# Kernel optimization log

Hardware: AMD Instinct MI355X
Metric: run time of the kernel (lower is better)

## Reference

```python
import jax, jax.numpy as jnp
import numpy as np

B, H, G, N, D, S, K = 1, 32, 128, 64, 128, 256, 8
BIT_PACK = 8


def setup_inputs() -> dict:
    key = jax.random.key(0)
    ks = jax.random.split(key, 6)
    data = jax.random.normal(ks[0], (B, H, G, N, D), dtype=jnp.float32)
    query = jax.random.normal(ks[1], (B, H, 1, D), dtype=jnp.float32)
    outlier_indices = jax.random.randint(ks[2], (B, H, G, K), 0, D, dtype=jnp.int32)
    norm_data = jax.random.uniform(ks[3], (B, H, G, N), dtype=jnp.float32)
    norm_outlier = jax.random.uniform(ks[4], (B, H, G, N), dtype=jnp.float32)
    # _init_proj_dir + _init_rot_dir (rot=True): per-chunk QR, scaled by sqrt(D)
    proj = np.asarray(jax.random.normal(ks[5], (D, S), dtype=jnp.float32), dtype=np.float64)
    num_chunks = (S + D - 1) // D
    qs = []
    for i in range(num_chunks):
        q, _ = np.linalg.qr(proj[:, i * D:(i + 1) * D])
        qs.append(q)
    proj_dir_score = jnp.asarray(np.concatenate(qs, axis=-1) * np.sqrt(D), dtype=jnp.float32)  # [D, S]
    proj_dir_quant = proj_dir_score.T  # [S, D]
    return {"data": data, "query": query, "outlier_indices": outlier_indices,
            "norm_data": norm_data, "norm_outlier": norm_outlier,
            "proj_dir_quant": proj_dir_quant, "proj_dir_score": proj_dir_score}


def _pack_bits(sketched):
    # sketched: [..., S] -> uint8 packed [..., S//8] ; bit = (sketched > 0)
    x = (sketched > 0).astype(jnp.int32).reshape(*sketched.shape[:-1], -1, BIT_PACK)
    enc = (2 ** jnp.arange(BIT_PACK, dtype=jnp.int32))
    return (x * enc).sum(axis=-1).astype(jnp.uint8)


def reference(data, query, outlier_indices, norm_data, norm_outlier, proj_dir_quant, proj_dir_score):
    s = proj_dir_quant.shape[0]
    d = data.shape[-1]
    # scatter outlier indices into a {0,1} mask over head_dim, per (B,H,G)
    mask = (jax.nn.one_hot(outlier_indices, d, dtype=jnp.float32).sum(axis=-2) > 0).astype(data.dtype)  # [B,H,G,D]
    key_outlier = data * mask[..., None, :]
    key_inlier = data * (1.0 - mask)[..., None, :]
    # JL random projection: [B,H,G,N,D] x [S,D] -> [B,H,G,N,S]
    sk_outlier = jnp.einsum('bhgnd,sd->bhgns', key_outlier, proj_dir_quant)
    sk_inlier = jnp.einsum('bhgnd,sd->bhgns', key_inlier, proj_dir_quant)
    # 1-bit sign quantization + byte packing
    hash_inlier = _pack_bits(sk_inlier)                  # [B,H,G,N,S//8]
    hash_outlier = _pack_bits(sk_outlier)[..., : s // 16]  # truncated outlier sketch
    # score path (PyTorch fallback math): inlier hamming-style inner product
    sketched_q = jnp.einsum('bhqd,ds->bhqs', query, proj_dir_score)[:, :, 0, :]  # [B,H,S]
    bits = jnp.where(sk_inlier > 0, 1.0, -1.0).astype(jnp.float32)  # == unpacked hash_inlier bits *2-1
    ip = jnp.einsum('bhs,bhgns->bhgn', sketched_q, bits)
    scl = jnp.sqrt(jnp.asarray(np.pi / 2, dtype=jnp.float32)) / s
    scores = (scl * norm_data * ip).reshape(data.shape[0], data.shape[1], -1, 1)  # [B,H,G*N,1]
    return hash_inlier, hash_outlier, scores
```

## Files before the change

### kernel.cpp

```cpp
#include <hip/hip_runtime.h>
#include <hip/hip_bf16.h>


typedef __attribute__((ext_vector_type(8))) short short8;
typedef __attribute__((ext_vector_type(4))) float f32x4;

constexpr int cH = 32, cG = 128, cN = 64, cD = 128, cS = 256, cK = 8;
constexpr int HASH_OUT_BASE = cH * cG * cN * (cS / 8);
constexpr int SCORE_BASE    = HASH_OUT_BASE + cH * cG * cN * (cS / 16);
constexpr float EPS_IN  = 1e-3f;
constexpr float EPS_OUT = 1e-3f;
constexpr size_t WS_BHI = 32768, WS_BLO = 98304, WS_NEED = 163840;

#define MFMA(a, b, c) __builtin_amdgcn_mfma_f32_16x16x32_bf16(a, b, c, 0, 0, 0)

__device__ inline short f2bf(float x) {
    unsigned u = __builtin_bit_cast(unsigned, x);
    u += 0x7FFFu + ((u >> 16) & 1u);
    return (short)(u >> 16);
}
__device__ inline float bf2f(short s) {
    return __builtin_bit_cast(float, (unsigned)((unsigned short)s) << 16);
}
__device__ inline unsigned long long sel4(unsigned long long a0, unsigned long long a1,
                                          unsigned long long a2, unsigned long long a3, int r) {
    unsigned long long x = a0;
    x = (r == 1) ? a1 : x; x = (r == 2) ? a2 : x; x = (r == 3) ? a3 : x;
    return x;
}
__device__ inline int sel8(const int* u, int k) {
    int x = u[0];
    x = (k == 1) ? u[1] : x; x = (k == 2) ? u[2] : x; x = (k == 3) ? u[3] : x;
    x = (k == 4) ? u[4] : x; x = (k == 5) ? u[5] : x; x = (k == 6) ? u[6] : x;
    x = (k == 7) ? u[7] : x;
    return x;
}
#define CE(i, j) { int a = u[i], b = u[j]; u[i] = min(a, b); u[j] = max(a, b); }

__device__ __attribute__((noinline)) float exact_inlier(
    const float* __restrict__ dr, const float* __restrict__ pr,
    unsigned long long m0, unsigned long long m1)
{
    float ex = 0.0f;
    #pragma unroll 1
    for (int dc = 0; dc < 4; ++dc) {
        float4 da[8], pa[8];
        #pragma unroll
        for (int j = 0; j < 8; ++j) {
            da[j] = reinterpret_cast<const float4*>(dr)[dc * 8 + j];
            pa[j] = reinterpret_cast<const float4*>(pr)[dc * 8 + j];
        }
        #pragma unroll
        for (int j = 0; j < 8; ++j) {
            float dv[4] = { da[j].x, da[j].y, da[j].z, da[j].w };
            float pv[4] = { pa[j].x, pa[j].y, pa[j].z, pa[j].w };
            #pragma unroll
            for (int e = 0; e < 4; ++e) {
                const int d = dc * 32 + j * 4 + e;
                const bool msk = ((((d < 64) ? (m0 >> d) : (m1 >> (d - 64))) & 1ull) != 0);
                ex = fmaf(dv[e], msk ? 0.0f : pv[e], ex);
            }
        }
    }
    return ex;
}

__global__ __launch_bounds__(256) void qjl_qv(
    const float* __restrict__ query, const float* __restrict__ projs,
    float* __restrict__ qv_out)
{
    const int h = blockIdx.x, s = threadIdx.x;
    float qa = 0.0f;
    for (int d = 0; d < cD; ++d)
        qa = fmaf(query[h * cD + d], projs[d * cS + s], qa);
    qv_out[h * cS + s] = qa;
}

__global__ __launch_bounds__(256) void qjl_bfrag(
    const float* __restrict__ projq, short* __restrict__ bhi, short* __restrict__ blo)
{
    const int idx = blockIdx.x * 256 + threadIdx.x;
    const int l = idx & 63, nt = (idx >> 6) & 15, ksub = idx >> 10;
    const int s = nt * 16 + (l & 15);
    const int k0 = ksub * 32 + (l >> 4) * 8;
    #pragma unroll
    for (int j = 0; j < 8; ++j) {
        float x = projq[s * cD + k0 + j];
        short h = f2bf(x);
        bhi[idx * 8 + j] = h;
        blo[idx * 8 + j] = f2bf(x - bf2f(h));
    }
}

__global__ __launch_bounds__(256, 3) void qjl_mfma(
    const float* __restrict__ data, const int* __restrict__ oidx,
    const float* __restrict__ norm_data, const float* __restrict__ projq,
    const float* __restrict__ qv_ws, const short* __restrict__ bhi_ws,
    const short* __restrict__ blo_ws, float* __restrict__ out)
{
    const int b    = blockIdx.x;
    const int t    = threadIdx.x;
    const int lane = t & 63;
    const int w    = t >> 6;
    const int c0   = lane & 15;
    const int g16  = lane >> 4;
    const int h    = b >> 7;

    __shared__ short A_hi[16 * 64 * 8];
    __shared__ short A_lo[16 * 64 * 8];
    __shared__ float dO[cK * cN];
    __shared__ float pO[cK * cS];
    __shared__ float ipPart[cN * 4];

    const f32x4 zero4 = { 0.f, 0.f, 0.f, 0.f };

    int u[cK];
    #pragma unroll
    for (int k = 0; k < cK; ++k) u[k] = oidx[b * cK + k];
    unsigned long long m0 = 0, m1 = 0;
    #pragma unroll
    for (int k = 0; k < cK; ++k) {
        int v = u[k];
        if (v < 64) m0 |= 1ull << v; else m1 |= 1ull << (v - 64);
    }
    CE(0,1) CE(2,3) CE(4,5) CE(6,7)
    CE(0,2) CE(1,3) CE(4,6) CE(5,7)
    CE(1,2) CE(5,6)
    CE(0,4) CE(1,5) CE(2,6) CE(3,7)
    CE(2,4) CE(3,5)
    CE(1,2) CE(3,4) CE(5,6)

    const float* __restrict__ chunk = data + (size_t)b * (cN * cD);

    #pragma unroll
    for (int i = 0; i < 4; ++i) {
        const int slot = i * 256 + t;
        const int l = slot & 63, frag = slot >> 6;
        const int mt = frag & 3, ksub = frag >> 2;
        const int row = mt * 16 + (l & 15);
        const int k0 = ksub * 32 + (l >> 4) * 8;
        const float4* p = reinterpret_cast<const float4*>(chunk + row * cD + k0);
        float4 v0 = p[0], v1 = p[1];
        float xs[8] = { v0.x, v0.y, v0.z, v0.w, v1.x, v1.y, v1.z, v1.w };
        const unsigned bits = (unsigned)(((k0 < 64) ? (m0 >> k0) : (m1 >> (k0 - 64))) & 0xFFull);
        short hs[8], ls[8];
        #pragma unroll
        for (int e = 0; e < 8; ++e) {
            float x = ((bits >> e) & 1u) ? 0.0f : xs[e];
            hs[e] = f2bf(x);
            ls[e] = f2bf(x - bf2f(hs[e]));
        }
        *reinterpret_cast<short8*>(&A_hi[slot * 8]) =
            short8{ hs[0], hs[1], hs[2], hs[3], hs[4], hs[5], hs[6], hs[7] };
        *reinterpret_cast<short8*>(&A_lo[slot * 8]) =
            short8{ ls[0], ls[1], ls[2], ls[3], ls[4], ls[5], ls[6], ls[7] };
    }
    #pragma unroll
    for (int i = 0; i < 2; ++i) {
        const int idx = i * 256 + t;
        const int k = idx >> 6, row = idx & 63;
        dO[idx] = chunk[row * cD + sel8(u, k)];
    }
    #pragma unroll
    for (int i = 0; i < 8; ++i) {
        const int idx = i * 256 + t;
        const int k = idx >> 8, s = idx & 255;
        const int uk = sel8(u, k);
        const bool dup = (k > 0) && (uk == sel8(u, k - 1));
        float x = projq[s * cD + uk];
        pO[idx] = dup ? 0.0f : x;
    }
    __syncthreads();

    if (w < 2) {
        short8 aO[4];
        #pragma unroll
        for (int mt = 0; mt < 4; ++mt) {
            short v8[8];
            #pragma unroll
            for (int k = 0; k < cK; ++k) {
                float x = dO[k * cN + mt * 16 + c0];
                short hi = f2bf(x), lo = f2bf(x - bf2f(hi));
                v8[k] = (g16 == 2) ? lo : ((g16 == 3) ? (short)0 : hi);
            }
            aO[mt] = short8{ v8[0], v8[1], v8[2], v8[3], v8[4], v8[5], v8[6], v8[7] };
        }
        short8 bO[4];
        #pragma unroll
        for (int q = 0; q < 4; ++q) {
            const int s = (w * 4 + q) * 16 + c0;
            short v8[8];
            #pragma unroll
            for (int k = 0; k < cK; ++k) {
                float x = pO[k * cS + s];
                short hi = f2bf(x), lo = f2bf(x - bf2f(hi));
                v8[k] = (g16 == 1) ? lo : ((g16 == 3) ? (short)0 : hi);
            }
            bO[q] = short8{ v8[0], v8[1], v8[2], v8[3], v8[4], v8[5], v8[6], v8[7] };
        }
        #pragma unroll
        for (int mt = 0; mt < 4; ++mt) {
            #pragma unroll
            for (int q = 0; q < 4; ++q) {
                f32x4 accO = MFMA(aO[mt], bO[q], zero4);
                unsigned long long b0, b1, b2, b3;
                #pragma unroll
                for (int r = 0; r < 4; ++r) {
                    float v = accO[r];
                    if (fabsf(v) < EPS_OUT) {
                        int row = mt * 16 + 4 * g16 + r;
                        int s = (w * 4 + q) * 16 + c0;
                        float o = 0.0f;
                        #pragma unroll
                        for (int k = 0; k < cK; ++k)
                            o = fmaf(dO[k * cN + row], pO[k * cS + s], o);
                        v = o;
                    }
                    unsigned long long bal = __ballot(v > 0.0f);
                    if (r == 0) b0 = bal; else if (r == 1) b1 = bal;
                    else if (r == 2) b2 = bal; else b3 = bal;
                }
                if (lane < 32) {
                    int r = lane & 3, g = (lane >> 2) & 3, hb = lane >> 4;
                    unsigned long long bb = sel4(b0, b1, b2, b3, r);
                    int row = mt * 16 + 4 * g + r;
                    out[HASH_OUT_BASE + (size_t)b * (cN * 16) + row * 16 + (w * 4 + q) * 2 + hb] =
                        (float)((bb >> (16 * g + 8 * hb)) & 0xFFull);
                }
            }
        }
    }

    f32x4 acc[16];
    #pragma unroll
    for (int i = 0; i < 16; ++i)
        acc[i] = zero4;

    #pragma unroll
    for (int ksub = 0; ksub < 4; ++ksub) {
        short8 ah[4], al[4];
        #pragma unroll
        for (int mt = 0; mt < 4; ++mt) {
            ah[mt] = *reinterpret_cast<const short8*>(&A_hi[((ksub * 4 + mt) * 64 + lane) * 8]);
            al[mt] = *reinterpret_cast<const short8*>(&A_lo[((ksub * 4 + mt) * 64 + lane) * 8]);
        }
        #pragma unroll
        for (int q = 0; q < 4; ++q) {
            short8 bh = *reinterpret_cast<const short8*>(
                &bhi_ws[((ksub * 16 + w * 4 + q) * 64 + lane) * 8]);
            #pragma unroll
            for (int mt = 0; mt < 4; ++mt)
                acc[mt * 4 + q] = MFMA(ah[mt], bh, acc[mt * 4 + q]);
            short8 bl = *reinterpret_cast<const short8*>(
                &blo_ws[((ksub * 16 + w * 4 + q) * 64 + lane) * 8]);
            #pragma unroll
            for (int mt = 0; mt < 4; ++mt)
                acc[mt * 4 + q] = MFMA(ah[mt], bl, acc[mt * 4 + q]);
            #pragma unroll
            for (int mt = 0; mt < 4; ++mt)
                acc[mt * 4 + q] = MFMA(al[mt], bh, acc[mt * 4 + q]);
        }
    }

    float qvv[4];
    #pragma unroll
    for (int q = 0; q < 4; ++q)
        qvv[q] = qv_ws[h * cS + (w * 4 + q) * 16 + c0];

    #pragma unroll
    for (int mt = 0; mt < 4; ++mt) {
        float part[4] = { 0.f, 0.f, 0.f, 0.f };
        #pragma unroll
        for (int q = 0; q < 4; ++q) {
            unsigned long long b0, b1, b2, b3;
            #pragma unroll
            for (int r = 0; r < 4; ++r) {
                float v = acc[mt * 4 + q][r];
                if (fabsf(v) < EPS_IN) {
                    int row = mt * 16 + 4 * g16 + r;
                    int s = (w * 4 + q) * 16 + c0;
                    v = exact_inlier(chunk + row * cD, projq + s * cD, m0, m1);
                }
                bool bit = v > 0.0f;
                unsigned long long bal = __ballot(bit);
                part[r] += bit ? qvv[q] : -qvv[q];
                if (r == 0) b0 = bal; else if (r == 1) b1 = bal;
                else if (r == 2) b2 = bal; else b3 = bal;
            }
            if (lane < 32) {
                int r = lane & 3, g = (lane >> 2) & 3, hb = lane >> 4;
                unsigned long long bb = sel4(b0, b1, b2, b3, r);
                int row = mt * 16 + 4 * g + r;
                out[(size_t)b * (cN * 32) + row * 32 + (w * 4 + q) * 2 + hb] =
                    (float)((bb >> (16 * g + 8 * hb)) & 0xFFull);
            }
        }
        #pragma unroll
        for (int r = 0; r < 4; ++r) {
            float x = part[r];
            x += __shfl_xor(x, 1); x += __shfl_xor(x, 2);
            x += __shfl_xor(x, 4); x += __shfl_xor(x, 8);
            if (c0 == 0) ipPart[(mt * 16 + 4 * g16 + r) * 4 + w] = x;
        }
    }
    __syncthreads();
    if (t < cN) {
        float ip = ipPart[t * 4 + 0] + ipPart[t * 4 + 1]
                 + ipPart[t * 4 + 2] + ipPart[t * 4 + 3];
        const float scl = 0.0048957583f;
        out[SCORE_BASE + (size_t)b * cN + t] = scl * norm_data[b * cN + t] * ip;
    }
}

__global__ __launch_bounds__(256) void qjl_valu(
    const float* __restrict__ data, const float* __restrict__ query,
    const int* __restrict__ oidx, const float* __restrict__ norm_data,
    const float* __restrict__ projq, const float* __restrict__ projs,
    float* __restrict__ out)
{
    const int b2 = blockIdx.x, b = b2 >> 1, half = b2 & 1;
    const int t = threadIdx.x, lane = t & 63, w = t >> 6, h = b >> 7;
    __shared__ float ipPart[32 * 4];
    int u[cK]; int U = 0;
    for (int k = 0; k < cK; ++k) {
        int v = oidx[b * cK + k];
        bool dup = false;
        for (int j = 0; j < U; ++j) dup = dup || (u[j] == v);
        if (!dup) u[U++] = v;
    }
    for (int i = 1; i < U; ++i) {
        int key = u[i], j = i - 1;
        while (j >= 0 && u[j] > key) { u[j + 1] = u[j]; --j; }
        u[j + 1] = key;
    }
    unsigned long long m0 = 0, m1 = 0;
    for (int k = 0; k < U; ++k) {
        int v = u[k];
        if (v < 64) m0 |= 1ull << v; else m1 |= 1ull << (v - 64);
    }
    int ui[cK]; float prO[cK];
    #pragma unroll
    for (int k = 0; k < cK; ++k) ui[k] = (k < U) ? u[k] : 0;
    #pragma unroll
    for (int k = 0; k < cK; ++k) prO[k] = (k < U) ? projq[t * cD + ui[k]] : 0.0f;
    float qv = 0.0f;
    for (int d = 0; d < cD; ++d)
        qv = fmaf(query[h * cD + d], projs[d * cS + t], qv);
    const float* __restrict__ chunk = data + (size_t)b * (cN * cD) + half * (32 * cD);
    float acc[32];
    #pragma unroll
    for (int n = 0; n < 32; ++n) acc[n] = 0.0f;
    for (int dc = 0; dc < cD / 16; ++dc) {
        float pm[16];
        const float4* p4 = reinterpret_cast<const float4*>(projq + t * cD + dc * 16);
        #pragma unroll
        for (int j = 0; j < 4; ++j) {
            float4 v = p4[j];
            float tmp[4] = { v.x, v.y, v.z, v.w };
            #pragma unroll
            for (int e = 0; e < 4; ++e) {
                int d = dc * 16 + j * 4 + e;
                bool msk = (((d < 64) ? (m0 >> d) : (m1 >> (d - 64))) & 1ull) != 0;
                pm[j * 4 + e] = msk ? 0.0f : tmp[e];
            }
        }
        #pragma unroll
        for (int n = 0; n < 32; ++n) {
            const float* __restrict__ r = chunk + n * cD + dc * 16;
            #pragma unroll
            for (int i = 0; i < 16; ++i)
                acc[n] = fmaf(r[i], pm[i], acc[n]);
        }
    }
    #pragma unroll
    for (int n = 0; n < 32; ++n) {
        const int nn = half * 32 + n;
        const float* __restrict__ r = chunk + n * cD;
        float o = 0.0f;
        #pragma unroll
        for (int k = 0; k < cK; ++k)
            o = fmaf((k < U) ? r[ui[k]] : 0.0f, prO[k], o);
        const bool bitIn = acc[n] > 0.0f;
        unsigned long long mIn = __ballot(bitIn);
        unsigned long long mOut = __ballot(o > 0.0f);
        float v = bitIn ? qv : -qv;
        #pragma unroll
        for (int off = 32; off > 0; off >>= 1) v += __shfl_down(v, off);
        if (lane == 0) ipPart[n * 4 + w] = v;
        if (lane < 8) {
            out[(size_t)b * (cN * 32) + nn * 32 + w * 8 + lane] =
                (float)((mIn >> (8 * lane)) & 0xFFull);
            if (w < 2)
                out[HASH_OUT_BASE + (size_t)b * (cN * 16) + nn * 16 + w * 8 + lane] =
                    (float)((mOut >> (8 * lane)) & 0xFFull);
        }
    }
    __syncthreads();
    if (t < 32) {
        float ip = ipPart[t * 4 + 0] + ipPart[t * 4 + 1] + ipPart[t * 4 + 2] + ipPart[t * 4 + 3];
        out[SCORE_BASE + b * cN + half * 32 + t] = 0.0048957583f * norm_data[b * cN + half * 32 + t] * ip;
    }
}

extern "C" void kernel_launch(void* const* d_in, const int* in_sizes, int n_in,
                              void* d_out, int out_size, void* d_ws, size_t ws_size,
                              hipStream_t stream) {
    const float* data      = (const float*)d_in[0];
    const float* query     = (const float*)d_in[1];
    const int*   oidx      = (const int*)d_in[2];
    const float* norm_data = (const float*)d_in[3];
    const float* projq     = (const float*)d_in[5];
    const float* projs     = (const float*)d_in[6];
    float* out = (float*)d_out;

    if (ws_size >= WS_NEED) {
        float* qv  = (float*)d_ws;
        short* bhi = (short*)((char*)d_ws + WS_BHI);
        short* blo = (short*)((char*)d_ws + WS_BLO);
        qjl_qv<<<cH, cS, 0, stream>>>(query, projs, qv);
        qjl_bfrag<<<16, 256, 0, stream>>>(projq, bhi, blo);
        qjl_mfma<<<cH * cG, 256, 0, stream>>>(data, oidx, norm_data, projq,
                                              qv, bhi, blo, out);
    } else {
        qjl_valu<<<cH * cG * 2, 256, 0, stream>>>(data, query, oidx, norm_data,
                                                  projq, projs, out);
    }
}
```

Before: 187.8 us.

## Split data bf16 conversion into a separate pass and read MFMA fragments from workspace

Adds a qjl_convert kernel that masks the data, splits it into hi/lo bf16 fragments in MFMA layout, and writes them plus the outlier columns to a large workspace. A new qjl_mfma2 kernel loads those fragments straight from global memory, without the LDS staging buffers, so LDS use drops and launch bounds rise to four blocks per CU. This costs an extra global round trip of about 130MB of fragment traffic and one more launch, and the new path runs only when the workspace is large enough. Otherwise it falls back to the old kernel.

```diff
diff --git a/kernel.cpp b/kernel.cpp
--- a/kernel.cpp
+++ b/kernel.cpp
@@ -10,7 +10,14 @@
 constexpr int SCORE_BASE    = HASH_OUT_BASE + cH * cG * cN * (cS / 16);
 constexpr float EPS_IN  = 1e-3f;
 constexpr float EPS_OUT = 1e-3f;
-constexpr size_t WS_BHI = 32768, WS_BLO = 98304, WS_NEED = 163840;
+constexpr size_t WS_QV  = 0;
+constexpr size_t WS_BHI = 32768;
+constexpr size_t WS_BLO = 98304;
+constexpr size_t WS_SMALL_NEED = 163840;
+constexpr size_t WS_AHI = 163840;
+constexpr size_t WS_ALO = WS_AHI + (size_t)4096 * 8192 * 2;
+constexpr size_t WS_DO  = WS_ALO + (size_t)4096 * 8192 * 2;
+constexpr size_t WS_BIG_NEED = WS_DO + (size_t)4096 * 512 * 4;
 
 #define MFMA(a, b, c) __builtin_amdgcn_mfma_f32_16x16x32_bf16(a, b, c, 0, 0, 0)
 
@@ -36,6 +43,23 @@
     return x;
 }
 #define CE(i, j) { int a = u[i], b = u[j]; u[i] = min(a, b); u[j] = max(a, b); }
+
+#define SORT8_AND_MASK(oidx_ptr, bb)                                   \
+    int u[cK];                                                         \
+    _Pragma("unroll")                                                  \
+    for (int k = 0; k < cK; ++k) u[k] = (oidx_ptr)[(bb) * cK + k];     \
+    unsigned long long m0 = 0, m1 = 0;                                 \
+    _Pragma("unroll")                                                  \
+    for (int k = 0; k < cK; ++k) {                                     \
+        int v = u[k];                                                  \
+        if (v < 64) m0 |= 1ull << v; else m1 |= 1ull << (v - 64);      \
+    }                                                                  \
+    CE(0,1) CE(2,3) CE(4,5) CE(6,7)                                    \
+    CE(0,2) CE(1,3) CE(4,6) CE(5,7)                                    \
+    CE(1,2) CE(5,6)                                                    \
+    CE(0,4) CE(1,5) CE(2,6) CE(3,7)                                    \
+    CE(2,4) CE(3,5)                                                    \
+    CE(1,2) CE(3,4) CE(5,6)
 
 __device__ __attribute__((noinline)) float exact_inlier(
     const float* __restrict__ dr, const float* __restrict__ pr,
@@ -89,6 +113,230 @@
         short h = f2bf(x);
         bhi[idx * 8 + j] = h;
         blo[idx * 8 + j] = f2bf(x - bf2f(h));
+    }
+}
+
+__global__ __launch_bounds__(256) void qjl_convert(
+    const float* __restrict__ data, const int* __restrict__ oidx,
+    short* __restrict__ ahi, short* __restrict__ alo, float* __restrict__ dOws)
+{
+    const int b = blockIdx.x;
+    const int t = threadIdx.x;
+    SORT8_AND_MASK(oidx, b)
+    const float* __restrict__ chunk = data + (size_t)b * (cN * cD);
+
+    #pragma unroll
+    for (int i = 0; i < 4; ++i) {
+        const int slot = i * 256 + t;
+        const int l = slot & 63, frag = slot >> 6;
+        const int mt = frag & 3, ksub = frag >> 2;
+        const int row = mt * 16 + (l & 15);
+        const int k0 = ksub * 32 + (l >> 4) * 8;
+        const float4* p = reinterpret_cast<const float4*>(chunk + row * cD + k0);
+        float4 v0 = p[0], v1 = p[1];
+        float xs[8] = { v0.x, v0.y, v0.z, v0.w, v1.x, v1.y, v1.z, v1.w };
+        const unsigned bits = (unsigned)(((k0 < 64) ? (m0 >> k0) : (m1 >> (k0 - 64))) & 0xFFull);
+        short hs[8], ls[8];
+        #pragma unroll
+        for (int e = 0; e < 8; ++e) {
+            float x = ((bits >> e) & 1u) ? 0.0f : xs[e];
+            hs[e] = f2bf(x);
+            ls[e] = f2bf(x - bf2f(hs[e]));
+        }
+        *reinterpret_cast<short8*>(&ahi[(size_t)b * 8192 + slot * 8]) =
+            short8{ hs[0], hs[1], hs[2], hs[3], hs[4], hs[5], hs[6], hs[7] };
+        *reinterpret_cast<short8*>(&alo[(size_t)b * 8192 + slot * 8]) =
+            short8{ ls[0], ls[1], ls[2], ls[3], ls[4], ls[5], ls[6], ls[7] };
+    }
+    #pragma unroll
+    for (int i = 0; i < 2; ++i) {
+        const int idx = i * 256 + t;
+        const int k = idx >> 6, row = idx & 63;
+        dOws[(size_t)b * 512 + idx] = chunk[row * cD + sel8(u, k)];
+    }
+}
+
+__global__ __launch_bounds__(256, 4) void qjl_mfma2(
+    const float* __restrict__ data, const int* __restrict__ oidx,
+    const float* __restrict__ norm_data, const float* __restrict__ projq,
+    const float* __restrict__ qv_ws, const short* __restrict__ bhi_ws,
+    const short* __restrict__ blo_ws, const short* __restrict__ ahi_ws,
+    const short* __restrict__ alo_ws, const float* __restrict__ dOws,
+    float* __restrict__ out)
+{
+    const int b    = blockIdx.x;
+    const int t    = threadIdx.x;
+    const int lane = t & 63;
+    const int w    = t >> 6;
+    const int c0   = lane & 15;
+    const int g16  = lane >> 4;
+    const int h    = b >> 7;
+
+    __shared__ float dO[cK * cN];
+    __shared__ float pO[cK * 128];
+    __shared__ float ipPart[cN * 4];
+
+    const f32x4 zero4 = { 0.f, 0.f, 0.f, 0.f };
+
+    SORT8_AND_MASK(oidx, b)
+    const float* __restrict__ chunk = data + (size_t)b * (cN * cD);
+
+    #pragma unroll
+    for (int i = 0; i < 2; ++i) {
+        const int idx = i * 256 + t;
+        dO[idx] = dOws[(size_t)b * 512 + idx];
+    }
+    #pragma unroll
+    for (int i = 0; i < 4; ++i) {
+        const int idx = i * 256 + t;
+        const int k = idx >> 7, s = idx & 127;
+        const int uk = sel8(u, k);
+        const bool dup = (k > 0) && (uk == sel8(u, k - 1));
+        float x = projq[s * cD + uk];
+        pO[idx] = dup ? 0.0f : x;
+    }
+    __syncthreads();
+
+    if (w < 2) {
+        short8 aO[4];
+        #pragma unroll
+        for (int mt = 0; mt < 4; ++mt) {
+            short v8[8];
+            #pragma unroll
+            for (int k = 0; k < cK; ++k) {
+                float x = dO[k * cN + mt * 16 + c0];
+                short hi = f2bf(x), lo = f2bf(x - bf2f(hi));
+                v8[k] = (g16 == 2) ? lo : ((g16 == 3) ? (short)0 : hi);
+            }
+            aO[mt] = short8{ v8[0], v8[1], v8[2], v8[3], v8[4], v8[5], v8[6], v8[7] };
+        }
+        short8 bO[4];
+        #pragma unroll
+        for (int q = 0; q < 4; ++q) {
+            const int s = (w * 4 + q) * 16 + c0;
+            short v8[8];
+            #pragma unroll
+            for (int k = 0; k < cK; ++k) {
+                float x = pO[k * 128 + s];
+                short hi = f2bf(x), lo = f2bf(x - bf2f(hi));
+                v8[k] = (g16 == 1) ? lo : ((g16 == 3) ? (short)0 : hi);
+            }
+            bO[q] = short8{ v8[0], v8[1], v8[2], v8[3], v8[4], v8[5], v8[6], v8[7] };
+        }
+        #pragma unroll
+        for (int mt = 0; mt < 4; ++mt) {
+            #pragma unroll
+            for (int q = 0; q < 4; ++q) {
+                f32x4 accO = MFMA(aO[mt], bO[q], zero4);
+                unsigned long long b0, b1, b2, b3;
+                #pragma unroll
+                for (int r = 0; r < 4; ++r) {
+                    float v = accO[r];
+                    if (fabsf(v) < EPS_OUT) {
+                        int row = mt * 16 + 4 * g16 + r;
+                        int s = (w * 4 + q) * 16 + c0;
+                        float o = 0.0f;
+                        #pragma unroll
+                        for (int k = 0; k < cK; ++k)
+                            o = fmaf(dO[k * cN + row], pO[k * 128 + s], o);
+                        v = o;
+                    }
+                    unsigned long long bal = __ballot(v > 0.0f);
+                    if (r == 0) b0 = bal; else if (r == 1) b1 = bal;
+                    else if (r == 2) b2 = bal; else b3 = bal;
+                }
+                if (lane < 32) {
+                    int r = lane & 3, g = (lane >> 2) & 3, hb = lane >> 4;
+                    unsigned long long bb = sel4(b0, b1, b2, b3, r);
+                    int row = mt * 16 + 4 * g + r;
+                    out[HASH_OUT_BASE + (size_t)b * (cN * 16) + row * 16 + (w * 4 + q) * 2 + hb] =
+                        (float)((bb >> (16 * g + 8 * hb)) & 0xFFull);
+                }
+            }
+        }
+    }
+
+    f32x4 acc[16];
+    #pragma unroll
+    for (int i = 0; i < 16; ++i)
+        acc[i] = zero4;
+
+    const short* __restrict__ aH = ahi_ws + (size_t)b * 8192;
+    const short* __restrict__ aL = alo_ws + (size_t)b * 8192;
+
+    #pragma unroll
+    for (int ksub = 0; ksub < 4; ++ksub) {
+        short8 ah[4], al[4];
+        #pragma unroll
+        for (int mt = 0; mt < 4; ++mt) {
+            ah[mt] = *reinterpret_cast<const short8*>(&aH[((ksub * 4 + mt) * 64 + lane) * 8]);
+            al[mt] = *reinterpret_cast<const short8*>(&aL[((ksub * 4 + mt) * 64 + lane) * 8]);
+        }
+        #pragma unroll
+        for (int q = 0; q < 4; ++q) {
+            short8 bh = *reinterpret_cast<const short8*>(
+                &bhi_ws[((ksub * 16 + w * 4 + q) * 64 + lane) * 8]);
+            #pragma unroll
+            for (int mt = 0; mt < 4; ++mt)
+                acc[mt * 4 + q] = MFMA(ah[mt], bh, acc[mt * 4 + q]);
+            short8 bl = *reinterpret_cast<const short8*>(
+                &blo_ws[((ksub * 16 + w * 4 + q) * 64 + lane) * 8]);
+            #pragma unroll
+            for (int mt = 0; mt < 4; ++mt)
+                acc[mt * 4 + q] = MFMA(ah[mt], bl, acc[mt * 4 + q]);
+            #pragma unroll
+            for (int mt = 0; mt < 4; ++mt)
+                acc[mt * 4 + q] = MFMA(al[mt], bh, acc[mt * 4 + q]);
+        }
+    }
+
+    float qvv[4];
+    #pragma unroll
+    for (int q = 0; q < 4; ++q)
+        qvv[q] = qv_ws[h * cS + (w * 4 + q) * 16 + c0];
+
+    #pragma unroll
+    for (int mt = 0; mt < 4; ++mt) {
+        float part[4] = { 0.f, 0.f, 0.f, 0.f };
+        #pragma unroll
+        for (int q = 0; q < 4; ++q) {
+            unsigned long long b0, b1, b2, b3;
+            #pragma unroll
+            for (int r = 0; r < 4; ++r) {
+                float v = acc[mt * 4 + q][r];
+                if (fabsf(v) < EPS_IN) {
+                    int row = mt * 16 + 4 * g16 + r;
+                    int s = (w * 4 + q) * 16 + c0;
+                    v = exact_inlier(chunk + row * cD, projq + s * cD, m0, m1);
+                }
+                bool bit = v > 0.0f;
+                unsigned long long bal = __ballot(bit);
+                part[r] += bit ? qvv[q] : -qvv[q];
+                if (r == 0) b0 = bal; else if (r == 1) b1 = bal;
+                else if (r == 2) b2 = bal; else b3 = bal;
+            }
+            if (lane < 32) {
+                int r = lane & 3, g = (lane >> 2) & 3, hb = lane >> 4;
+                unsigned long long bb = sel4(b0, b1, b2, b3, r);
+                int row = mt * 16 + 4 * g + r;
+                out[(size_t)b * (cN * 32) + row * 32 + (w * 4 + q) * 2 + hb] =
+                    (float)((bb >> (16 * g + 8 * hb)) & 0xFFull);
+            }
+        }
+        #pragma unroll
+        for (int r = 0; r < 4; ++r) {
+            float x = part[r];
+            x += __shfl_xor(x, 1); x += __shfl_xor(x, 2);
+            x += __shfl_xor(x, 4); x += __shfl_xor(x, 8);
+            if (c0 == 0) ipPart[(mt * 16 + 4 * g16 + r) * 4 + w] = x;
+        }
+    }
+    __syncthreads();
+    if (t < cN) {
+        float ip = ipPart[t * 4 + 0] + ipPart[t * 4 + 1]
+                 + ipPart[t * 4 + 2] + ipPart[t * 4 + 3];
+        const float scl = 0.0048957583f;
+        out[SCORE_BASE + (size_t)b * cN + t] = scl * norm_data[b * cN + t] * ip;
     }
 }
 
@@ -114,22 +362,7 @@
 
     const f32x4 zero4 = { 0.f, 0.f, 0.f, 0.f };
 
-    int u[cK];
-    #pragma unroll
-    for (int k = 0; k < cK; ++k) u[k] = oidx[b * cK + k];
-    unsigned long long m0 = 0, m1 = 0;
-    #pragma unroll
-    for (int k = 0; k < cK; ++k) {
-        int v = u[k];
-        if (v < 64) m0 |= 1ull << v; else m1 |= 1ull << (v - 64);
-    }
-    CE(0,1) CE(2,3) CE(4,5) CE(6,7)
-    CE(0,2) CE(1,3) CE(4,6) CE(5,7)
-    CE(1,2) CE(5,6)
-    CE(0,4) CE(1,5) CE(2,6) CE(3,7)
-    CE(2,4) CE(3,5)
-    CE(1,2) CE(3,4) CE(5,6)
-
+    SORT8_AND_MASK(oidx, b)
     const float* __restrict__ chunk = data + (size_t)b * (cN * cD);
 
     #pragma unroll
@@ -413,8 +646,20 @@
     const float* projs     = (const float*)d_in[6];
     float* out = (float*)d_out;
 
-    if (ws_size >= WS_NEED) {
-        float* qv  = (float*)d_ws;
+    if (ws_size >= WS_BIG_NEED) {
+        float* qv  = (float*)((char*)d_ws + WS_QV);
+        short* bhi = (short*)((char*)d_ws + WS_BHI);
+        short* blo = (short*)((char*)d_ws + WS_BLO);
+        short* ahi = (short*)((char*)d_ws + WS_AHI);
+        short* alo = (short*)((char*)d_ws + WS_ALO);
+        float* dOw = (float*)((char*)d_ws + WS_DO);
+        qjl_qv<<<cH, cS, 0, stream>>>(query, projs, qv);
+        qjl_bfrag<<<16, 256, 0, stream>>>(projq, bhi, blo);
+        qjl_convert<<<cH * cG, 256, 0, stream>>>(data, oidx, ahi, alo, dOw);
+        qjl_mfma2<<<cH * cG, 256, 0, stream>>>(data, oidx, norm_data, projq,
+                                               qv, bhi, blo, ahi, alo, dOw, out);
+    } else if (ws_size >= WS_SMALL_NEED) {
+        float* qv  = (float*)((char*)d_ws + WS_QV);
         short* bhi = (short*)((char*)d_ws + WS_BHI);
         short* blo = (short*)((char*)d_ws + WS_BLO);
         qjl_qv<<<cH, cS, 0, stream>>>(query, projs, qv);
```

Result: slower. 369.8 us (+96.9%).
